# Kernel tuning notes

Measured on AMD Instinct MI355X. Metric: run time of the kernel, lower is better.

Reference implementation:

```python
import jax, jax.numpy as jnp
import numpy as np

# ---- db6 filter bank (pywt conventions) ----
_REC_LO = np.array([0.11154074335008017, 0.4946238903983854, 0.7511339080215775,
                    0.3152503517092432, -0.22626469396516913, -0.12976686756709563,
                    0.09750160558707936, 0.02752286553001629, -0.031582039318031156,
                    0.0005538422009938016, 0.004777257511010651, -0.00107730108499558],
                   dtype=np.float32)
_REC_HI = _REC_LO[::-1].copy(); _REC_HI[1::2] *= -1.0          # qmf(rec_lo)
_DEC_LO = _REC_LO[::-1].copy()
_DEC_HI = _REC_HI[::-1].copy()
L = 12          # filter length
LEVEL = 8       # J
# pytorch_wavelets cross-correlates with dec[::-1] == true conv with dec.
# lax.conv_general_dilated is correlation, so analysis kernels = dec[::-1] = rec filters.
ANA = jnp.asarray(np.stack([_REC_LO, _REC_HI])[:, None, :])     # [2,1,L]
SYN = jnp.asarray(np.stack([_DEC_LO, _DEC_HI])[None, :, :])     # [1,2,L]


def dwt1d(x, J):
    """Multi-level DWT, mode='symmetric'. x: [B,C,N] -> (yl [B,C,m], [yh1..yhJ])."""
    B, C, N = x.shape
    lo = x.reshape(B * C, 1, N)
    highs = []
    for _ in range(J):
        n = lo.shape[-1]
        outlen = (n + L - 1) // 2                    # pywt dwt_coeff_len
        p = 2 * (outlen - 1) - n + L
        xp = jnp.pad(lo, ((0, 0), (0, 0), (p // 2, (p + 1) // 2)), mode='symmetric')
        y = jax.lax.conv_general_dilated(xp, ANA, (2,), 'VALID',
                                         dimension_numbers=('NCH', 'OIH', 'NCH'))
        lo = y[:, :1]
        highs.append(y[:, 1:].reshape(B, C, outlen))
    return lo.reshape(B, C, -1), highs


def idwt1d(yl, yhs):
    """Inverse of dwt1d. yl: [B,C,m], yhs list (level1..levelJ)."""
    B, C, _ = yl.shape
    lo = yl.reshape(B * C, 1, -1)
    pad = L - 1 - (L - 2)                            # torch convT padding L-2 -> lax pad 1
    for h in yhs[::-1]:
        h = h.reshape(B * C, 1, -1)
        if lo.shape[-1] > h.shape[-1]:               # 'unpad' extra sample
            lo = lo[..., :h.shape[-1]]
        xh = jnp.concatenate([lo, h], axis=1)        # [BC,2,n]
        lo = jax.lax.conv_general_dilated(xh, SYN, (1,), [(pad, pad)],
                                          lhs_dilation=(2,),
                                          dimension_numbers=('NCH', 'OIH', 'NCH'))
    return lo.reshape(B, C, -1)


def wno_forward(x, fc0_w, fc0_b, w1, w2, cw, cb, fc1_w, fc1_b, fc2_w, fc2_b):
    B, s, _ = x.shape
    grid = jnp.broadcast_to(jnp.linspace(0.0, 1.0, s, dtype=x.dtype)[None, :, None], (B, s, 1))
    v = jnp.concatenate([x, grid], axis=-1) @ fc0_w + fc0_b     # [B,s,W]
    v = v.transpose(0, 2, 1)                                     # [B,W,s]
    n_layers = w1.shape[0]
    for i in range(n_layers):
        yl, yhs = dwt1d(v, LEVEL)
        yl = jnp.einsum('bix,iox->box', yl, w1[i])               # mix approx coeffs
        yhs[-1] = jnp.einsum('bix,iox->box', yhs[-1], w2[i])     # mix finest-level detail
        x1 = idwt1d(yl, yhs)
        x2 = jnp.einsum('bis,io->bos', v, cw[i]) + cb[i][None, :, None]  # 1x1 conv
        v = x1 + x2
        if i < n_layers - 1:
            v = jax.nn.gelu(v, approximate=False)
    v = v.transpose(0, 2, 1)
    v = jax.nn.gelu(v @ fc1_w + fc1_b, approximate=False)
    return v @ fc2_w + fc2_b                                     # [B,s,1]


def setup_inputs() -> dict:
    key = jax.random.key(0)
    B, S, W, NL = 32, 8192, 64, 4
    n = S
    for _ in range(LEVEL):
        n = (n + L - 1) // 2
    modes = n                                                    # 42
    ks = jax.random.split(key, 12)
    scale = 1.0 / (W * W)
    return {
        'x': jax.random.normal(ks[0], (B, S, 1), jnp.float32),
        'fc0_w': jax.random.normal(ks[1], (2, W), jnp.float32) * 0.5,
        'fc0_b': jax.random.normal(ks[2], (W,), jnp.float32) * 0.1,
        'w1': scale * jax.random.uniform(ks[3], (NL, W, W, modes), jnp.float32),
        'w2': scale * jax.random.uniform(ks[4], (NL, W, W, modes), jnp.float32),
        'cw': jax.random.normal(ks[5], (NL, W, W), jnp.float32) * (1.0 / np.sqrt(W)),
        'cb': jax.random.normal(ks[6], (NL, W), jnp.float32) * 0.05,
        'fc1_w': jax.random.normal(ks[7], (W, 128), jnp.float32) * (1.0 / np.sqrt(W)),
        'fc1_b': jax.random.normal(ks[8], (128,), jnp.float32) * 0.05,
        'fc2_w': jax.random.normal(ks[9], (128, 1), jnp.float32) * (1.0 / np.sqrt(128.0)),
        'fc2_b': jax.random.normal(ks[10], (1,), jnp.float32) * 0.05,
    }


def reference(x, fc0_w, fc0_b, w1, w2, cw, cb, fc1_w, fc1_b, fc2_w, fc2_b):
    return wno_forward(x, fc0_w, fc0_b, w1, w2, cw, cb, fc1_w, fc1_b, fc2_w, fc2_b)
```

## Files before the change

### kernel.cpp

```cpp
#include <hip/hip_runtime.h>
#include <cmath>

#define BC 2048
#define S_LEN 8192
#define MODES 42
#define HTOT 8248
#define LO_STR 1036

static constexpr float C_LO[12] = {
  0.11154074335008017f, 0.4946238903983854f, 0.7511339080215775f,
  0.3152503517092432f, -0.22626469396516913f, -0.12976686756709563f,
  0.09750160558707936f, 0.02752286553001629f, -0.031582039318031156f,
  0.0005538422009938016f, 0.004777257511010651f, -0.00107730108499558f };

__device__ __forceinline__ float rec_lo_c(int k){ return C_LO[k]; }
__device__ __forceinline__ float rec_hi_c(int k){ float v = C_LO[11-k]; return (k&1)? -v : v; }
__device__ __forceinline__ float dec_lo_c(int k){ return C_LO[11-k]; }
__device__ __forceinline__ float dec_hi_c(int k){ float v = C_LO[k];    return (k&1)?  v : -v; }

__device__ __forceinline__ float erf_fast(float x){
  float ax = fabsf(x);
  float t  = __fdividef(1.0f, 1.0f + 0.3275911f * ax);
  float p  = ((((1.061405429f * t - 1.453152027f) * t) + 1.421413741f) * t - 0.284496736f) * t + 0.254829592f;
  float y  = 1.0f - p * t * __expf(-ax * ax);
  return copysignf(y, x);
}
__device__ __forceinline__ float gelu_f(float x){
  return 0.5f * x * (1.0f + erf_fast(x * 0.70710678118654752440f));
}

__device__ __forceinline__ int reflect_i(int t, int n){
  t = (t < 0) ? (-1 - t) : t;
  t = (t >= n) ? (2 * n - 1 - t) : t;
  return t;
}

__device__ __forceinline__ unsigned short bf16_rn(float x){
  unsigned int b = __float_as_uint(x);
  b += 0x7FFF + ((b >> 16) & 1);
  return (unsigned short)(b >> 16);
}
__device__ __forceinline__ float bf16_to_f(unsigned short h){
  return __uint_as_float(((unsigned int)h) << 16);
}

typedef short  v8s __attribute__((ext_vector_type(8)));
typedef float  v4f __attribute__((ext_vector_type(4)));
typedef unsigned short u16;

__device__ __forceinline__ void ld3f4(float* w, const float* s){
  *(float4*)&w[0] = *(const float4*)&s[0];
  *(float4*)&w[4] = *(const float4*)&s[4];
  *(float4*)&w[8] = *(const float4*)&s[8];
}
__device__ __forceinline__ void ld5f4(float* w, const float* s){
  *(float4*)&w[0]  = *(const float4*)&s[0];
  *(float4*)&w[4]  = *(const float4*)&s[4];
  *(float4*)&w[8]  = *(const float4*)&s[8];
  *(float4*)&w[12] = *(const float4*)&s[12];
  *(float4*)&w[16] = *(const float4*)&s[16];
}

__device__ __forceinline__ void stage_g(float* dst, const float* src, int g0, int cnt, int n){
  for (int j4 = threadIdx.x; j4 < (cnt >> 2); j4 += 256) {
    int g = g0 + 4 * j4;
    float4 val;
    if (g >= 0 && g + 3 < n) val = *(const float4*)&src[g];
    else {
      val.x = (g   >= 0 && g   < n) ? src[g]   : 0.f;
      val.y = (g+1 >= 0 && g+1 < n) ? src[g+1] : 0.f;
      val.z = (g+2 >= 0 && g+2 < n) ? src[g+2] : 0.f;
      val.w = (g+3 >= 0 && g+3 < n) ? src[g+3] : 0.f;
    }
    *(float4*)&dst[4*j4] = val;
  }
}

template<int OFF>
__device__ __forceinline__ float idwt_tap(const float* wl, const float* wh, int d){
  float acc = 0.f;
  int t = OFF + (d >> 1);
  if (d & 1) {
    #pragma unroll
    for (int i = 0; i < 6; ++i) acc += wl[t+i]*dec_lo_c(2*i)   + wh[t+i]*dec_hi_c(2*i);
  } else {
    #pragma unroll
    for (int i = 0; i < 6; ++i) acc += wl[t+i]*dec_lo_c(2*i+1) + wh[t+i]*dec_hi_c(2*i+1);
  }
  return acc;
}

__global__ __launch_bounds__(256) void prep_split(
    const float* __restrict__ fc1w, const float* __restrict__ cw,
    u16* __restrict__ whH, u16* __restrict__ whL,
    u16* __restrict__ wcH, u16* __restrict__ wcL)
{
  int i = blockIdx.x * 256 + threadIdx.x;
  if (i < 8192) {
    int c = i >> 7, j = i & 127;
    float wv = fc1w[i];
    u16 h = bf16_rn(wv);
    float lo = wv - bf16_to_f(h);
    int cs = c ^ ((j & 7) << 3);
    whH[j * 64 + cs] = h; whL[j * 64 + cs] = bf16_rn(lo);
  }
  int k = i - 8192;
  if (k >= 0 && k < 16384) {
    int l = k >> 12, r = k & 4095;
    int c = r >> 6, o = r & 63;
    float wv = cw[k];
    u16 h = bf16_rn(wv);
    float lo = wv - bf16_to_f(h);
    int cs = c ^ ((o & 7) << 3);
    wcH[l * 4096 + o * 64 + cs] = h; wcL[l * 4096 + o * 64 + cs] = bf16_rn(lo);
  }
}

__global__ __launch_bounds__(256) void fc0_kernel(
    const float* __restrict__ x, const float* __restrict__ w,
    const float* __restrict__ bias, float* __restrict__ v)
{
  int p = blockIdx.x * 256 + threadIdx.x;
  int b = p >> 13, s = p & 8191;
  float xv = x[p];
  float g  = (float)s * (1.0f / 8191.0f);
  for (int c = 0; c < 64; ++c) {
    v[((size_t)(b * 64 + c)) * S_LEN + s] = xv * w[c] + g * w[64 + c] + bias[c];
  }
}

__global__ __launch_bounds__(256) void dwt_big(
    const float* __restrict__ vin, float* __restrict__ highs, float* __restrict__ lo_f)
{
  __shared__ alignas(16) float sV[2184], sL1[1088], sL2[544];
  int seq = blockIdx.x >> 2, c = blockIdx.x & 3;
  const float* src = vin + (size_t)seq * S_LEN;
  float* hseq = highs + (size_t)seq * HTOT;
  int tid = threadIdx.x;

  int g0 = 2080 * c - 72;
  for (int j4 = tid; j4 < 545; j4 += 256) {
    int g = g0 + 4 * j4;
    float4 val;
    if (g >= 0 && g + 3 < 8192) val = *(const float4*)&src[g];
    else {
      val.x = src[reflect_i(g,   8192)];
      val.y = src[reflect_i(g+1, 8192)];
      val.z = src[reflect_i(g+2, 8192)];
      val.w = src[reflect_i(g+3, 8192)];
    }
    *(float4*)&sV[4*j4] = val;
  }
  __syncthreads();

  int base1 = 1040 * c - 30;
  for (int u0 = 4*tid; u0 < 1082; u0 += 1024) {
    float w[20];
    ld5f4(w, &sV[2*u0]);
    #pragma unroll
    for (int d = 0; d < 4; ++d) {
      if (u0 + d < 1082) {
        float alo = 0.f, ahi = 0.f;
        #pragma unroll
        for (int k = 0; k < 12; ++k) {
          float x = w[2*d + 2 + k];
          alo += x * rec_lo_c(k); ahi += x * rec_hi_c(k);
        }
        sL1[u0+d] = alo;
        int m1 = base1 + u0 + d;
        if (m1 >= 1040*c && m1 < 1040*c + 1040 && m1 >= 0 && m1 < 4101) hseq[m1] = ahi;
      }
    }
  }
  __syncthreads();
  if (c == 0) { for (int u = tid;        u < 30;   u += 256) sL1[u] = sL1[59 - u]; }
  if (c == 3) { for (int u = 1011 + tid; u < 1082; u += 256) sL1[u] = sL1[2021 - u]; }
  __syncthreads();

  int base2 = 520 * c - 10;
  for (int u0 = 4*tid; u0 < 534; u0 += 1024) {
    float w[20];
    ld5f4(w, &sL1[2*u0]);
    #pragma unroll
    for (int d = 0; d < 4; ++d) {
      if (u0 + d < 534) {
        float alo = 0.f, ahi = 0.f;
        #pragma unroll
        for (int k = 0; k < 12; ++k) {
          float x = w[2*d + k];
          alo += x * rec_lo_c(k); ahi += x * rec_hi_c(k);
        }
        sL2[u0+d] = alo;
        int m2 = base2 + u0 + d;
        if (m2 >= 520*c && m2 < 520*c + 520 && m2 >= 0 && m2 < 2056) hseq[4104 + m2] = ahi;
      }
    }
  }
  __syncthreads();
  if (c == 0) { for (int u = tid;       u < 10;  u += 256) sL2[u] = sL2[19 - u]; }
  if (c == 3) { for (int u = 506 + tid; u < 534; u += 256) sL2[u] = sL2[1011 - u]; }
  __syncthreads();

  for (int u0 = 4*tid; u0 < 260; u0 += 1024) {
    float w[20];
    ld5f4(w, &sL2[2*u0]);
    #pragma unroll
    for (int d = 0; d < 4; ++d) {
      int m3 = 260*c + u0 + d;
      if (u0 + d < 260 && m3 < 1033) {
        float alo = 0.f, ahi = 0.f;
        #pragma unroll
        for (int k = 0; k < 12; ++k) {
          float x = w[2*d + k];
          alo += x * rec_lo_c(k); ahi += x * rec_hi_c(k);
        }
        lo_f[(size_t)seq * LO_STR + m3] = alo;
        hseq[6160 + m3] = ahi;
      }
    }
  }
}

__device__ __forceinline__ void dwt_lvl_v(const float* in, int n, float* out, int outn, float* hg)
{
  for (int u0 = 4*(int)threadIdx.x; u0 < outn; u0 += 1024) {
    bool fast = (u0 >= 8) && (2*u0 + 7 < n) && (u0 + 3 < outn);
    if (fast) {
      float w[20];
      ld5f4(w, &in[2*u0 - 12]);
      #pragma unroll
      for (int d = 0; d < 4; ++d) {
        float alo = 0.f, ahi = 0.f;
        #pragma unroll
        for (int k = 0; k < 12; ++k) {
          float x = w[2*d + 2 + k];
          alo += x * rec_lo_c(k); ahi += x * rec_hi_c(k);
        }
        out[u0+d] = alo; hg[u0+d] = ahi;
      }
    } else {
      for (int d = 0; d < 4; ++d) {
        if (u0 + d < outn) {
          float alo = 0.f, ahi = 0.f;
          #pragma unroll
          for (int k = 0; k < 12; ++k) {
            float x = in[reflect_i(2*(u0+d) + k - 10, n)];
            alo += x * rec_lo_c(k); ahi += x * rec_hi_c(k);
          }
          out[u0+d] = alo; hg[u0+d] = ahi;
        }
      }
    }
  }
  __syncthreads();
}

__global__ __launch_bounds__(256) void dwt_small(
    const float* __restrict__ lo_f, float* __restrict__ highs, float* __restrict__ yl)
{
  __shared__ alignas(16) float A[1040], Bb[528];
  int seq = blockIdx.x;
  const float* src = lo_f + (size_t)seq * LO_STR;
  float* hseq = highs + (size_t)seq * HTOT;
  for (int i = 4*(int)threadIdx.x; i < 1033; i += 1024) {
    if (i + 3 < 1033) *(float4*)&A[i] = *(const float4*)&src[i];
    else { for (int d = 0; d < 4; ++d) if (i + d < 1033) A[i+d] = src[i+d]; }
  }
  __syncthreads();
  dwt_lvl_v(A, 1033, Bb, 522, hseq + 7196);
  dwt_lvl_v(Bb, 522, A, 266, hseq + 7720);
  dwt_lvl_v(A, 266, Bb, 138, hseq + 7988);
  dwt_lvl_v(Bb, 138, A, 74,  hseq + 8128);
  dwt_lvl_v(A, 74,  Bb, 42,  hseq + 8204);
  for (int m = threadIdx.x; m < MODES; m += 256) yl[seq * MODES + m] = Bb[m];
}

__global__ __launch_bounds__(256) void mix2(
    const float* __restrict__ yl_raw, const float* __restrict__ highs,
    const float* __restrict__ w1i, const float* __restrict__ w2i,
    float* __restrict__ yl_m, float* __restrict__ yh_m)
{
  bool hi = blockIdx.x >= 336;
  int idx = (blockIdx.x - (hi ? 336 : 0)) * 256 + threadIdx.x;
  if (idx >= 32 * 64 * MODES) return;
  int xx = idx % MODES;
  int o  = (idx / MODES) % 64;
  int b  = idx / (MODES * 64);
  const float* in = hi ? (highs + 8204) : yl_raw;
  size_t stride   = hi ? HTOT : MODES;
  const float* w  = hi ? w2i : w1i;
  float acc = 0.f;
  for (int i = 0; i < 64; ++i)
    acc += in[((size_t)(b * 64 + i)) * stride + xx] * w[(i * 64 + o) * MODES + xx];
  (hi ? yh_m : yl_m)[(b * 64 + o) * MODES + xx] = acc;
}

__device__ __forceinline__ void idwt_lvl8(const float* lo, const float* h, float* out, int outn)
{
  for (int u0 = 8*(int)threadIdx.x; u0 < outn; u0 += 2048) {
    int ib = u0 >> 1;
    float wl[12], wh[12];
    ld3f4(wl, &lo[ib]); ld3f4(wh, &h[ib]);
    #pragma unroll
    for (int d = 0; d < 8; ++d)
      if (u0 + d < outn) out[u0+d] = idwt_tap<0>(wl, wh, d);
  }
  __syncthreads();
}

__device__ __forceinline__ void stage_band(float* dst, const float* src, int len, int alloc)
{
  for (int i = threadIdx.x; i < alloc; i += 256) dst[i] = (i < len) ? src[i] : 0.f;
}

__global__ __launch_bounds__(256) void idwt_small(
    const float* __restrict__ yl_m, const float* __restrict__ yh_m,
    const float* __restrict__ highs, float* __restrict__ lo_i)
{
  __shared__ alignas(16) float bands[1120], wa[272], wb[528];
  int seq = blockIdx.x;
  const float* hseq = highs + (size_t)seq * HTOT;
  stage_band(bands + 0,   yl_m + (size_t)seq * MODES, 42, 48);
  stage_band(bands + 48,  yh_m + (size_t)seq * MODES, 42, 48);
  stage_band(bands + 96,  hseq + 8128, 74, 80);
  stage_band(bands + 176, hseq + 7988, 138, 144);
  stage_band(bands + 320, hseq + 7720, 266, 272);
  stage_band(bands + 592, hseq + 7196, 522, 528);
  __syncthreads();
  idwt_lvl8(bands + 0,  bands + 48,  wa, 74);
  idwt_lvl8(wa,         bands + 96,  wb, 138);
  idwt_lvl8(wb,         bands + 176, wa, 266);
  idwt_lvl8(wa,         bands + 320, wb, 522);
  for (int u0 = 8*(int)threadIdx.x; u0 < 1033; u0 += 2048) {
    int ib = u0 >> 1;
    float wl[12], wh[12];
    ld3f4(wl, &wb[ib]); ld3f4(wh, &bands[592 + ib]);
    float o[8];
    #pragma unroll
    for (int d = 0; d < 8; ++d) o[d] = idwt_tap<0>(wl, wh, d);
    float* dst = lo_i + (size_t)seq * LO_STR + u0;
    if (u0 + 7 < 1033) {
      *(float4*)&dst[0] = make_float4(o[0], o[1], o[2], o[3]);
      *(float4*)&dst[4] = make_float4(o[4], o[5], o[6], o[7]);
    } else {
      for (int d = 0; d < 8; ++d) if (u0 + d < 1033) dst[d] = o[d];
    }
  }
}

__global__ __launch_bounds__(256) void idwt_big(
    const float* __restrict__ lo_i, const float* __restrict__ highs, float* __restrict__ x1)
{
  __shared__ alignas(16) float sL3[288], sH3[288], sL2[544], sH2[544], sL1[1048], sH1[1048];
  int seq = blockIdx.x >> 2, c = blockIdx.x & 3;
  const float* hseq = highs + (size_t)seq * HTOT;
  const float* l3   = lo_i + (size_t)seq * LO_STR;
  int g3 = 256*c - 4, g2 = 512*c - 4, g1 = 1024*c - 4;

  stage_g(sL3, l3,          g3, 288, 1033);
  stage_g(sH3, hseq + 6160, g3, 288, 1033);
  stage_g(sH2, hseq + 4104, g2, 544, 2056);
  stage_g(sH1, hseq,        g1, 1048, 4101);
  __syncthreads();

  for (int u0 = 8*(int)threadIdx.x; u0 < 536; u0 += 2048) {
    int ib = u0 >> 1;
    float wl[12], wh[12];
    ld3f4(wl, &sL3[ib]); ld3f4(wh, &sH3[ib]);
    #pragma unroll
    for (int d = 0; d < 8; ++d) {
      if (u0 + d < 536) {
        int m = 512*c - 2 + u0 + d;
        float acc = idwt_tap<3>(wl, wh, d);
        sL2[u0 + d + 2] = (m >= 0 && m < 2056) ? acc : 0.f;
      }
    }
  }
  __syncthreads();

  for (int u0 = 8*(int)threadIdx.x; u0 < 1040; u0 += 2048) {
    int ib = u0 >> 1;
    float wl[12], wh[12];
    ld3f4(wl, &sL2[ib]); ld3f4(wh, &sH2[ib]);
    #pragma unroll
    for (int d = 0; d < 8; ++d) {
      if (u0 + d < 1040) {
        int m = 1024*c - 2 + u0 + d;
        float acc = idwt_tap<3>(wl, wh, d);
        sL1[u0 + d + 2] = (m >= 0 && m < 4101) ? acc : 0.f;
      }
    }
  }
  __syncthreads();

  {
    int u0 = 8*(int)threadIdx.x;
    int ib = (u0 >> 1) + 4;
    float wl[12], wh[12];
    ld3f4(wl, &sL1[ib]); ld3f4(wh, &sH1[ib]);
    float o[8];
    #pragma unroll
    for (int d = 0; d < 8; ++d) o[d] = idwt_tap<0>(wl, wh, d);
    float* dst = x1 + (size_t)seq * S_LEN + 2048*c + u0;
    *(float4*)&dst[0] = make_float4(o[0], o[1], o[2], o[3]);
    *(float4*)&dst[4] = make_float4(o[4], o[5], o[6], o[7]);
  }
}

__global__ __launch_bounds__(256) void pw_mfma(
    const float* __restrict__ x1, float* v,
    const u16* __restrict__ wcH, const u16* __restrict__ wcL,
    const float* __restrict__ cb, int do_gelu)
{
  __shared__ u16 aH[64][64], aL[64][64];
  __shared__ u16 wH[64][64], wL[64][64];
  __shared__ float cbl[64];
  int b  = blockIdx.x >> 7;
  int s0 = (blockIdx.x & 127) << 6;
  int t  = threadIdx.x;

  {
    const v8s* srcH = (const v8s*)wcH;
    const v8s* srcL = (const v8s*)wcL;
    v8s* dstH = (v8s*)&wH[0][0];
    v8s* dstL = (v8s*)&wL[0][0];
    #pragma unroll
    for (int r = 0; r < 2; ++r) {
      dstH[t + 256 * r] = srcH[t + 256 * r];
      dstL[t + 256 * r] = srcL[t + 256 * r];
    }
  }
  if (t < 64) cbl[t] = cb[t];

  #pragma unroll
  for (int r = 0; r < 4; ++r) {
    int idx = t + 256 * r;
    int ch = idx >> 4, p4 = (idx & 15) << 2;
    float4 xv = *(const float4*)&v[((size_t)(b * 64 + ch)) * S_LEN + s0 + p4];
    u16 h0 = bf16_rn(xv.x); aH[p4+0][ch ^ (((p4+0)&7)<<3)] = h0; aL[p4+0][ch ^ (((p4+0)&7)<<3)] = bf16_rn(xv.x - bf16_to_f(h0));
    u16 h1 = bf16_rn(xv.y); aH[p4+1][ch ^ (((p4+1)&7)<<3)] = h1; aL[p4+1][ch ^ (((p4+1)&7)<<3)] = bf16_rn(xv.y - bf16_to_f(h1));
    u16 h2 = bf16_rn(xv.z); aH[p4+2][ch ^ (((p4+2)&7)<<3)] = h2; aL[p4+2][ch ^ (((p4+2)&7)<<3)] = bf16_rn(xv.z - bf16_to_f(h2));
    u16 h3 = bf16_rn(xv.w); aH[p4+3][ch ^ (((p4+3)&7)<<3)] = h3; aL[p4+3][ch ^ (((p4+3)&7)<<3)] = bf16_rn(xv.w - bf16_to_f(h3));
  }
  __syncthreads();

  int l = t & 63, wv_ = t >> 6;
  int pi = l & 15, kg = l >> 4;
  int pos = wv_ * 16 + pi;
  int swz = (pi & 7) << 3;

  v4f acc[4];
  #pragma unroll
  for (int i = 0; i < 4; ++i) acc[i] = v4f{0.f, 0.f, 0.f, 0.f};

  #pragma unroll
  for (int kt = 0; kt < 2; ++kt) {
    int ka = (kg * 8 + kt * 32) ^ swz;
    v8s ah = *(const v8s*)&aH[pos][ka];
    v8s al = *(const v8s*)&aL[pos][ka];
    #pragma unroll
    for (int ct = 0; ct < 4; ++ct) {
      int o = ct * 16 + pi;
      v8s bh = *(const v8s*)&wH[o][ka];
      v8s bl = *(const v8s*)&wL[o][ka];
      acc[ct] = __builtin_amdgcn_mfma_f32_16x16x32_bf16(ah, bh, acc[ct], 0, 0, 0);
      acc[ct] = __builtin_amdgcn_mfma_f32_16x16x32_bf16(ah, bl, acc[ct], 0, 0, 0);
      acc[ct] = __builtin_amdgcn_mfma_f32_16x16x32_bf16(al, bh, acc[ct], 0, 0, 0);
    }
  }

  #pragma unroll
  for (int ct = 0; ct < 4; ++ct) {
    int o = ct * 16 + pi;
    size_t base = ((size_t)(b * 64 + o)) * S_LEN + s0 + wv_ * 16 + kg * 4;
    float4 x4 = *(const float4*)&x1[base];
    float cbv = cbl[o];
    float y0 = acc[ct][0] + x4.x + cbv;
    float y1 = acc[ct][1] + x4.y + cbv;
    float y2 = acc[ct][2] + x4.z + cbv;
    float y3 = acc[ct][3] + x4.w + cbv;
    if (do_gelu) { y0 = gelu_f(y0); y1 = gelu_f(y1); y2 = gelu_f(y2); y3 = gelu_f(y3); }
    float4 y4 = make_float4(y0, y1, y2, y3);
    *(float4*)&v[base] = y4;
  }
}

__global__ __launch_bounds__(256) void head_mfma(
    const float* __restrict__ v,
    const u16* __restrict__ whH, const u16* __restrict__ whL,
    const float* __restrict__ fc1b, const float* __restrict__ fc2w,
    const float* __restrict__ fc2b, float* __restrict__ out)
{
  __shared__ u16 aH[64][64], aL[64][64];
  __shared__ u16 wH[128][64], wL[128][64];
  __shared__ float f1b[128], f2w[128];
  int b  = blockIdx.x >> 7;
  int s0 = (blockIdx.x & 127) << 6;
  int t  = threadIdx.x;

  {
    const v8s* srcH = (const v8s*)whH;
    const v8s* srcL = (const v8s*)whL;
    v8s* dstH = (v8s*)&wH[0][0];
    v8s* dstL = (v8s*)&wL[0][0];
    #pragma unroll
    for (int r = 0; r < 4; ++r) {
      dstH[t + 256 * r] = srcH[t + 256 * r];
      dstL[t + 256 * r] = srcL[t + 256 * r];
    }
  }
  if (t < 128) { f1b[t] = fc1b[t]; f2w[t] = fc2w[t]; }

  #pragma unroll
  for (int r = 0; r < 4; ++r) {
    int idx = t + 256 * r;
    int ch = idx >> 4, p4 = (idx & 15) << 2;
    float4 xv = *(const float4*)&v[((size_t)(b * 64 + ch)) * S_LEN + s0 + p4];
    u16 h0 = bf16_rn(xv.x); aH[p4+0][ch ^ (((p4+0)&7)<<3)] = h0; aL[p4+0][ch ^ (((p4+0)&7)<<3)] = bf16_rn(xv.x - bf16_to_f(h0));
    u16 h1 = bf16_rn(xv.y); aH[p4+1][ch ^ (((p4+1)&7)<<3)] = h1; aL[p4+1][ch ^ (((p4+1)&7)<<3)] = bf16_rn(xv.y - bf16_to_f(h1));
    u16 h2 = bf16_rn(xv.z); aH[p4+2][ch ^ (((p4+2)&7)<<3)] = h2; aL[p4+2][ch ^ (((p4+2)&7)<<3)] = bf16_rn(xv.z - bf16_to_f(h2));
    u16 h3 = bf16_rn(xv.w); aH[p4+3][ch ^ (((p4+3)&7)<<3)] = h3; aL[p4+3][ch ^ (((p4+3)&7)<<3)] = bf16_rn(xv.w - bf16_to_f(h3));
  }
  __syncthreads();

  int l = t & 63, wv_ = t >> 6;
  int pi = l & 15, kg = l >> 4;
  int pos = wv_ * 16 + pi;
  int swz = (pi & 7) << 3;

  v4f acc[8];
  #pragma unroll
  for (int i = 0; i < 8; ++i) acc[i] = v4f{0.f, 0.f, 0.f, 0.f};

  #pragma unroll
  for (int kt = 0; kt < 2; ++kt) {
    int ka = (kg * 8 + kt * 32) ^ swz;
    v8s ah = *(const v8s*)&aH[pos][ka];
    v8s al = *(const v8s*)&aL[pos][ka];
    #pragma unroll
    for (int ct = 0; ct < 8; ++ct) {
      int j = ct * 16 + pi;
      v8s bh = *(const v8s*)&wH[j][ka];
      v8s bl = *(const v8s*)&wL[j][ka];
      acc[ct] = __builtin_amdgcn_mfma_f32_16x16x32_bf16(ah, bh, acc[ct], 0, 0, 0);
      acc[ct] = __builtin_amdgcn_mfma_f32_16x16x32_bf16(ah, bl, acc[ct], 0, 0, 0);
      acc[ct] = __builtin_amdgcn_mfma_f32_16x16x32_bf16(al, bh, acc[ct], 0, 0, 0);
    }
  }

  float part[4] = {0.f, 0.f, 0.f, 0.f};
  #pragma unroll
  for (int ct = 0; ct < 8; ++ct) {
    int j = ct * 16 + pi;
    float bias = f1b[j], f2 = f2w[j];
    #pragma unroll
    for (int r = 0; r < 4; ++r) {
      float d = acc[ct][r] + bias;
      part[r] += f2 * gelu_f(d);
    }
  }
  #pragma unroll
  for (int r = 0; r < 4; ++r) {
    part[r] += __shfl_xor(part[r], 1, 16);
    part[r] += __shfl_xor(part[r], 2, 16);
    part[r] += __shfl_xor(part[r], 4, 16);
    part[r] += __shfl_xor(part[r], 8, 16);
  }
  if (pi == 0) {
    float b2 = fc2b[0];
    float4 o4 = make_float4(part[0] + b2, part[1] + b2, part[2] + b2, part[3] + b2);
    *(float4*)&out[(size_t)b * S_LEN + s0 + wv_ * 16 + kg * 4] = o4;
  }
}

extern "C" void kernel_launch(void* const* d_in, const int* in_sizes, int n_in,
                              void* d_out, int out_size, void* d_ws, size_t ws_size,
                              hipStream_t stream) {
  const float* x    = (const float*)d_in[0];
  const float* fc0w = (const float*)d_in[1];
  const float* fc0b = (const float*)d_in[2];
  const float* w1   = (const float*)d_in[3];
  const float* w2   = (const float*)d_in[4];
  const float* cw   = (const float*)d_in[5];
  const float* cb   = (const float*)d_in[6];
  const float* fc1w = (const float*)d_in[7];
  const float* fc1b = (const float*)d_in[8];
  const float* fc2w = (const float*)d_in[9];
  const float* fc2b = (const float*)d_in[10];
  float* out = (float*)d_out;

  float* ws     = (float*)d_ws;
  float* v      = ws;
  float* x1     = v      + (size_t)BC * S_LEN;
  float* highs  = x1     + (size_t)BC * S_LEN;
  float* yl_raw = highs  + (size_t)BC * HTOT;
  float* yl_m   = yl_raw + (size_t)BC * MODES;
  float* yh_m   = yl_m   + (size_t)BC * MODES;
  float* lo_f   = yh_m   + (size_t)BC * MODES;
  float* lo_i   = lo_f   + (size_t)BC * LO_STR;
  u16*   whH    = (u16*)(lo_i + (size_t)BC * LO_STR);
  u16*   whL    = whH + 8192;
  u16*   wcH    = whL + 8192;
  u16*   wcL    = wcH + 16384;
  size_t needed = (size_t)((char*)(wcL + 16384) - (char*)ws);
  if (ws_size < needed) return;

  prep_split<<<96, 256, 0, stream>>>(fc1w, cw, whH, whL, wcH, wcL);
  fc0_kernel<<<1024, 256, 0, stream>>>(x, fc0w, fc0b, v);

  for (int i = 0; i < 4; ++i) {
    dwt_big<<<BC * 4, 256, 0, stream>>>(v, highs, lo_f);
    dwt_small<<<BC, 256, 0, stream>>>(lo_f, highs, yl_raw);
    mix2<<<672, 256, 0, stream>>>(yl_raw, highs, w1 + (size_t)i * 64 * 64 * MODES,
                                  w2 + (size_t)i * 64 * 64 * MODES, yl_m, yh_m);
    idwt_small<<<BC, 256, 0, stream>>>(yl_m, yh_m, highs, lo_i);
    idwt_big<<<BC * 4, 256, 0, stream>>>(lo_i, highs, x1);
    pw_mfma<<<4096, 256, 0, stream>>>(x1, v, wcH + i * 4096, wcL + i * 4096, cb + i * 64, (i < 3) ? 1 : 0);
  }

  head_mfma<<<4096, 256, 0, stream>>>(v, whH, whL, fc1b, fc2w, fc2b, out);
}
```

Before: 610.1 us.

## Fuse mode mixing into idwt_small and deinterleave DWT shared buffers

The separate mix2 kernel goes away. Its per-mode channel contraction is now done inside idwt_small, with each block computing its own output channel's 42 low and high modes before the inverse transform. dwt_big now keeps even and odd samples in separate shared arrays, so strided filter reads become contiguous vector loads, and it writes high bands with float4 stores. The idwt kernels drop from 8 to 4 outputs per thread to cut register pressure. The fused mixing work runs on only 42 threads per block and re-reads weights for every (b,o), which may serialize or add global traffic.

```diff
diff --git a/kernel.cpp b/kernel.cpp
--- a/kernel.cpp
+++ b/kernel.cpp
@@ -59,6 +59,12 @@
   *(float4*)&w[8]  = *(const float4*)&s[8];
   *(float4*)&w[12] = *(const float4*)&s[12];
   *(float4*)&w[16] = *(const float4*)&s[16];
+}
+__device__ __forceinline__ void ld4f2(float* w, const float* s){
+  *(float2*)&w[0] = *(const float2*)&s[0];
+  *(float2*)&w[2] = *(const float2*)&s[2];
+  *(float2*)&w[4] = *(const float2*)&s[4];
+  *(float2*)&w[6] = *(const float2*)&s[6];
 }
 
 __device__ __forceinline__ void stage_g(float* dst, const float* src, int g0, int cnt, int n){
@@ -76,18 +82,36 @@
   }
 }
 
-template<int OFF>
-__device__ __forceinline__ float idwt_tap(const float* wl, const float* wh, int d){
-  float acc = 0.f;
-  int t = OFF + (d >> 1);
-  if (d & 1) {
-    #pragma unroll
-    for (int i = 0; i < 6; ++i) acc += wl[t+i]*dec_lo_c(2*i)   + wh[t+i]*dec_hi_c(2*i);
-  } else {
-    #pragma unroll
-    for (int i = 0; i < 6; ++i) acc += wl[t+i]*dec_lo_c(2*i+1) + wh[t+i]*dec_hi_c(2*i+1);
-  }
-  return acc;
+__device__ __forceinline__ void stage_band4(float* dst, const float* src, int len, int alloc){
+  for (int i4 = threadIdx.x; i4 < (alloc >> 2); i4 += 256) {
+    int i = 4 * i4;
+    float4 v;
+    if (i + 3 < len) v = *(const float4*)&src[i];
+    else {
+      v.x = (i   < len) ? src[i]   : 0.f;
+      v.y = (i+1 < len) ? src[i+1] : 0.f;
+      v.z = (i+2 < len) ? src[i+2] : 0.f;
+      v.w = (i+3 < len) ? src[i+3] : 0.f;
+    }
+    *(float4*)&dst[i] = v;
+  }
+}
+
+template<int SH>
+__device__ __forceinline__ void idwt4s(const float* wl, const float* wh, float* o4){
+  #pragma unroll
+  for (int d = 0; d < 4; ++d) {
+    const int q = SH + (d >> 1);
+    float acc = 0.f;
+    if (d & 1) {
+      #pragma unroll
+      for (int i = 0; i < 6; ++i) acc += wl[q+i]*dec_lo_c(2*i)   + wh[q+i]*dec_hi_c(2*i);
+    } else {
+      #pragma unroll
+      for (int i = 0; i < 6; ++i) acc += wl[q+i]*dec_lo_c(2*i+1) + wh[q+i]*dec_hi_c(2*i+1);
+    }
+    o4[d] = acc;
+  }
 }
 
 __global__ __launch_bounds__(256) void prep_split(
@@ -132,13 +156,18 @@
 __global__ __launch_bounds__(256) void dwt_big(
     const float* __restrict__ vin, float* __restrict__ highs, float* __restrict__ lo_f)
 {
-  __shared__ alignas(16) float sV[2184], sL1[1088], sL2[544];
+  __shared__ alignas(16) float sVE[1096], sVO[1096];
+  __shared__ alignas(16) float sL1Eb[548], sL1Ob[548];
+  __shared__ alignas(16) float sL2E[276], sL2O[276];
+  float* sL1E = sL1Eb + 4;
+  float* sL1O = sL1Ob + 4;
+
   int seq = blockIdx.x >> 2, c = blockIdx.x & 3;
   const float* src = vin + (size_t)seq * S_LEN;
   float* hseq = highs + (size_t)seq * HTOT;
   int tid = threadIdx.x;
 
-  int g0 = 2080 * c - 72;
+  int g0 = 2080 * c - 76;
   for (int j4 = tid; j4 < 545; j4 += 256) {
     int g = g0 + 4 * j4;
     float4 val;
@@ -149,73 +178,127 @@
       val.z = src[reflect_i(g+2, 8192)];
       val.w = src[reflect_i(g+3, 8192)];
     }
-    *(float4*)&sV[4*j4] = val;
-  }
-  __syncthreads();
-
-  int base1 = 1040 * c - 30;
-  for (int u0 = 4*tid; u0 < 1082; u0 += 1024) {
-    float w[20];
-    ld5f4(w, &sV[2*u0]);
-    #pragma unroll
-    for (int d = 0; d < 4; ++d) {
-      if (u0 + d < 1082) {
+    *(float2*)&sVE[2*j4] = make_float2(val.x, val.z);
+    *(float2*)&sVO[2*j4] = make_float2(val.y, val.w);
+  }
+  __syncthreads();
+
+  {
+    int base1m = 1040 * c - 32;
+    int uh1 = (c < 3) ? 1072 : 1013;
+    for (int u0 = 4 * tid; u0 < 1084; u0 += 1024) {
+      float we[12], wo[12];
+      ld3f4(we, &sVE[u0]); ld3f4(wo, &sVO[u0]);
+      float lo4[4], hi4[4];
+      #pragma unroll
+      for (int d = 0; d < 4; ++d) {
         float alo = 0.f, ahi = 0.f;
         #pragma unroll
-        for (int k = 0; k < 12; ++k) {
-          float x = w[2*d + 2 + k];
-          alo += x * rec_lo_c(k); ahi += x * rec_hi_c(k);
+        for (int j = 0; j < 6; ++j) {
+          float e = we[d+1+j], oo = wo[d+1+j];
+          alo += e * rec_lo_c(2*j) + oo * rec_lo_c(2*j+1);
+          ahi += e * rec_hi_c(2*j) + oo * rec_hi_c(2*j+1);
         }
-        sL1[u0+d] = alo;
-        int m1 = base1 + u0 + d;
-        if (m1 >= 1040*c && m1 < 1040*c + 1040 && m1 >= 0 && m1 < 4101) hseq[m1] = ahi;
+        lo4[d] = alo; hi4[d] = ahi;
       }
-    }
-  }
-  __syncthreads();
-  if (c == 0) { for (int u = tid;        u < 30;   u += 256) sL1[u] = sL1[59 - u]; }
-  if (c == 3) { for (int u = 1011 + tid; u < 1082; u += 256) sL1[u] = sL1[2021 - u]; }
-  __syncthreads();
-
-  int base2 = 520 * c - 10;
-  for (int u0 = 4*tid; u0 < 534; u0 += 1024) {
-    float w[20];
-    ld5f4(w, &sL1[2*u0]);
-    #pragma unroll
-    for (int d = 0; d < 4; ++d) {
-      if (u0 + d < 534) {
+      *(float2*)&sL1E[u0 >> 1] = make_float2(lo4[0], lo4[2]);
+      *(float2*)&sL1O[u0 >> 1] = make_float2(lo4[1], lo4[3]);
+      if (u0 >= 32 && u0 + 3 < uh1) {
+        *(float4*)&hseq[base1m + u0] = make_float4(hi4[0], hi4[1], hi4[2], hi4[3]);
+      } else {
+        #pragma unroll
+        for (int d = 0; d < 4; ++d) {
+          int u = u0 + d;
+          if (u >= 32 && u < uh1) hseq[base1m + u] = hi4[d];
+        }
+      }
+    }
+  }
+  __syncthreads();
+  if (c == 0) {
+    for (int u = tid; u < 32; u += 256) {
+      int j = 63 - u;
+      float v = (j & 1) ? sL1O[j >> 1] : sL1E[j >> 1];
+      if (u & 1) sL1O[u >> 1] = v; else sL1E[u >> 1] = v;
+    }
+  }
+  if (c == 3) {
+    for (int u = 1013 + tid; u < 1084; u += 256) {
+      int j = 2025 - u;
+      float v = (j & 1) ? sL1O[j >> 1] : sL1E[j >> 1];
+      if (u & 1) sL1O[u >> 1] = v; else sL1E[u >> 1] = v;
+    }
+  }
+  __syncthreads();
+
+  {
+    int base2m = 520 * c - 12;
+    int uh2 = (c < 3) ? 532 : 508;
+    for (int u0 = 4 * tid; u0 < 536; u0 += 1024) {
+      float we[12], wo[12];
+      ld3f4(we, &sL1E[u0 - 4]); ld3f4(wo, &sL1O[u0 - 4]);
+      float lo4[4], hi4[4];
+      #pragma unroll
+      for (int d = 0; d < 4; ++d) {
         float alo = 0.f, ahi = 0.f;
         #pragma unroll
-        for (int k = 0; k < 12; ++k) {
-          float x = w[2*d + k];
-          alo += x * rec_lo_c(k); ahi += x * rec_hi_c(k);
+        for (int j = 0; j < 6; ++j) {
+          float e = we[d+3+j], oo = wo[d+3+j];
+          alo += e * rec_lo_c(2*j) + oo * rec_lo_c(2*j+1);
+          ahi += e * rec_hi_c(2*j) + oo * rec_hi_c(2*j+1);
         }
-        sL2[u0+d] = alo;
-        int m2 = base2 + u0 + d;
-        if (m2 >= 520*c && m2 < 520*c + 520 && m2 >= 0 && m2 < 2056) hseq[4104 + m2] = ahi;
+        lo4[d] = alo; hi4[d] = ahi;
       }
-    }
-  }
-  __syncthreads();
-  if (c == 0) { for (int u = tid;       u < 10;  u += 256) sL2[u] = sL2[19 - u]; }
-  if (c == 3) { for (int u = 506 + tid; u < 534; u += 256) sL2[u] = sL2[1011 - u]; }
-  __syncthreads();
-
-  for (int u0 = 4*tid; u0 < 260; u0 += 1024) {
-    float w[20];
-    ld5f4(w, &sL2[2*u0]);
+      *(float2*)&sL2E[u0 >> 1] = make_float2(lo4[0], lo4[2]);
+      *(float2*)&sL2O[u0 >> 1] = make_float2(lo4[1], lo4[3]);
+      if (u0 >= 12 && u0 < uh2)
+        *(float4*)&hseq[4104 + base2m + u0] = make_float4(hi4[0], hi4[1], hi4[2], hi4[3]);
+    }
+  }
+  __syncthreads();
+  if (c == 0) {
+    for (int u = tid; u < 12; u += 256) {
+      int j = 23 - u;
+      float v = (j & 1) ? sL2O[j >> 1] : sL2E[j >> 1];
+      if (u & 1) sL2O[u >> 1] = v; else sL2E[u >> 1] = v;
+    }
+  }
+  if (c == 3) {
+    for (int u = 508 + tid; u < 536; u += 256) {
+      int j = 1015 - u;
+      float v = (j & 1) ? sL2O[j >> 1] : sL2E[j >> 1];
+      if (u & 1) sL2O[u >> 1] = v; else sL2E[u >> 1] = v;
+    }
+  }
+  __syncthreads();
+
+  for (int u0 = 4 * tid; u0 < 260; u0 += 1024) {
+    float we[12], wo[12];
+    ld3f4(we, &sL2E[u0]); ld3f4(wo, &sL2O[u0]);
+    float lo4[4], hi4[4];
     #pragma unroll
     for (int d = 0; d < 4; ++d) {
-      int m3 = 260*c + u0 + d;
-      if (u0 + d < 260 && m3 < 1033) {
-        float alo = 0.f, ahi = 0.f;
-        #pragma unroll
-        for (int k = 0; k < 12; ++k) {
-          float x = w[2*d + k];
-          alo += x * rec_lo_c(k); ahi += x * rec_hi_c(k);
+      float alo = 0.f, ahi = 0.f;
+      #pragma unroll
+      for (int j = 0; j < 6; ++j) {
+        float e = we[d+1+j], oo = wo[d+1+j];
+        alo += e * rec_lo_c(2*j) + oo * rec_lo_c(2*j+1);
+        ahi += e * rec_hi_c(2*j) + oo * rec_hi_c(2*j+1);
+      }
+      lo4[d] = alo; hi4[d] = ahi;
+    }
+    int m0 = 260 * c + u0;
+    if (m0 + 3 < 1033) {
+      *(float4*)&lo_f[(size_t)seq * LO_STR + m0] = make_float4(lo4[0], lo4[1], lo4[2], lo4[3]);
+      *(float4*)&hseq[6160 + m0] = make_float4(hi4[0], hi4[1], hi4[2], hi4[3]);
+    } else {
+      #pragma unroll
+      for (int d = 0; d < 4; ++d) {
+        int m = m0 + d;
+        if (m < 1033 && u0 + d < 260) {
+          lo_f[(size_t)seq * LO_STR + m] = lo4[d];
+          hseq[6160 + m] = hi4[d];
         }
-        lo_f[(size_t)seq * LO_STR + m3] = alo;
-        hseq[6160 + m3] = ahi;
       }
     }
   }
@@ -275,76 +358,64 @@
   for (int m = threadIdx.x; m < MODES; m += 256) yl[seq * MODES + m] = Bb[m];
 }
 
-__global__ __launch_bounds__(256) void mix2(
+__device__ __forceinline__ void idwt_lvl4(const float* lo, const float* h, float* out, int outn)
+{
+  for (int u0 = 4*(int)threadIdx.x; u0 < outn; u0 += 1024) {
+    int q = u0 >> 1;
+    float wl[8], wh[8];
+    ld4f2(wl, &lo[q]); ld4f2(wh, &h[q]);
+    float o4[4]; idwt4s<0>(wl, wh, o4);
+    if (u0 + 3 < outn) *(float4*)&out[u0] = make_float4(o4[0], o4[1], o4[2], o4[3]);
+    else { for (int d = 0; d < 4; ++d) if (u0 + d < outn) out[u0+d] = o4[d]; }
+  }
+  __syncthreads();
+}
+
+__global__ __launch_bounds__(256) void idwt_small(
     const float* __restrict__ yl_raw, const float* __restrict__ highs,
-    const float* __restrict__ w1i, const float* __restrict__ w2i,
-    float* __restrict__ yl_m, float* __restrict__ yh_m)
-{
-  bool hi = blockIdx.x >= 336;
-  int idx = (blockIdx.x - (hi ? 336 : 0)) * 256 + threadIdx.x;
-  if (idx >= 32 * 64 * MODES) return;
-  int xx = idx % MODES;
-  int o  = (idx / MODES) % 64;
-  int b  = idx / (MODES * 64);
-  const float* in = hi ? (highs + 8204) : yl_raw;
-  size_t stride   = hi ? HTOT : MODES;
-  const float* w  = hi ? w2i : w1i;
-  float acc = 0.f;
-  for (int i = 0; i < 64; ++i)
-    acc += in[((size_t)(b * 64 + i)) * stride + xx] * w[(i * 64 + o) * MODES + xx];
-  (hi ? yh_m : yl_m)[(b * 64 + o) * MODES + xx] = acc;
-}
-
-__device__ __forceinline__ void idwt_lvl8(const float* lo, const float* h, float* out, int outn)
-{
-  for (int u0 = 8*(int)threadIdx.x; u0 < outn; u0 += 2048) {
-    int ib = u0 >> 1;
-    float wl[12], wh[12];
-    ld3f4(wl, &lo[ib]); ld3f4(wh, &h[ib]);
-    #pragma unroll
-    for (int d = 0; d < 8; ++d)
-      if (u0 + d < outn) out[u0+d] = idwt_tap<0>(wl, wh, d);
-  }
-  __syncthreads();
-}
-
-__device__ __forceinline__ void stage_band(float* dst, const float* src, int len, int alloc)
-{
-  for (int i = threadIdx.x; i < alloc; i += 256) dst[i] = (i < len) ? src[i] : 0.f;
-}
-
-__global__ __launch_bounds__(256) void idwt_small(
-    const float* __restrict__ yl_m, const float* __restrict__ yh_m,
-    const float* __restrict__ highs, float* __restrict__ lo_i)
+    const float* __restrict__ w1l, const float* __restrict__ w2l,
+    float* __restrict__ lo_i)
 {
   __shared__ alignas(16) float bands[1120], wa[272], wb[528];
   int seq = blockIdx.x;
+  int b = seq >> 6, o = seq & 63;
   const float* hseq = highs + (size_t)seq * HTOT;
-  stage_band(bands + 0,   yl_m + (size_t)seq * MODES, 42, 48);
-  stage_band(bands + 48,  yh_m + (size_t)seq * MODES, 42, 48);
-  stage_band(bands + 96,  hseq + 8128, 74, 80);
-  stage_band(bands + 176, hseq + 7988, 138, 144);
-  stage_band(bands + 320, hseq + 7720, 266, 272);
-  stage_band(bands + 592, hseq + 7196, 522, 528);
-  __syncthreads();
-  idwt_lvl8(bands + 0,  bands + 48,  wa, 74);
-  idwt_lvl8(wa,         bands + 96,  wb, 138);
-  idwt_lvl8(wb,         bands + 176, wa, 266);
-  idwt_lvl8(wa,         bands + 320, wb, 522);
-  for (int u0 = 8*(int)threadIdx.x; u0 < 1033; u0 += 2048) {
-    int ib = u0 >> 1;
-    float wl[12], wh[12];
-    ld3f4(wl, &wb[ib]); ld3f4(wh, &bands[592 + ib]);
-    float o[8];
-    #pragma unroll
-    for (int d = 0; d < 8; ++d) o[d] = idwt_tap<0>(wl, wh, d);
+  int t = threadIdx.x;
+
+  stage_band4(bands + 96,  hseq + 8128, 74, 80);
+  stage_band4(bands + 176, hseq + 7988, 138, 144);
+  stage_band4(bands + 320, hseq + 7720, 266, 272);
+  stage_band4(bands + 592, hseq + 7196, 522, 528);
+
+  if (t >= 42 && t < 48) { bands[t] = 0.f; bands[48 + t] = 0.f; }
+  if (t < 42) {
+    const float* yr = yl_raw + (size_t)b * 2688 + t;
+    const float* hh = highs + (size_t)(b * 64) * HTOT + 8204 + t;
+    const float* wl = w1l + o * 42 + t;
+    const float* wh = w2l + o * 42 + t;
+    float accl = 0.f, acch = 0.f;
+    #pragma unroll 4
+    for (int i = 0; i < 64; ++i) {
+      accl += yr[i * 42] * wl[i * 2688];
+      acch += hh[(size_t)i * HTOT] * wh[i * 2688];
+    }
+    bands[t] = accl; bands[48 + t] = acch;
+  }
+  __syncthreads();
+
+  idwt_lvl4(bands + 0,   bands + 48,  wa, 74);
+  idwt_lvl4(wa,          bands + 96,  wb, 138);
+  idwt_lvl4(wb,          bands + 176, wa, 266);
+  idwt_lvl4(wa,          bands + 320, wb, 522);
+
+  for (int u0 = 4 * t; u0 < 1033; u0 += 1024) {
+    int q = u0 >> 1;
+    float wl[8], wh[8];
+    ld4f2(wl, &wb[q]); ld4f2(wh, &bands[592 + q]);
+    float o4[4]; idwt4s<0>(wl, wh, o4);
     float* dst = lo_i + (size_t)seq * LO_STR + u0;
-    if (u0 + 7 < 1033) {
-      *(float4*)&dst[0] = make_float4(o[0], o[1], o[2], o[3]);
-      *(float4*)&dst[4] = make_float4(o[4], o[5], o[6], o[7]);
-    } else {
-      for (int d = 0; d < 8; ++d) if (u0 + d < 1033) dst[d] = o[d];
-    }
+    if (u0 + 3 < 1033) *(float4*)&dst[0] = make_float4(o4[0], o4[1], o4[2], o4[3]);
+    else { for (int d = 0; d < 4; ++d) if (u0 + d < 1033) dst[d] = o4[d]; }
   }
 }
 
@@ -356,6 +427,7 @@
   const float* hseq = highs + (size_t)seq * HTOT;
   const float* l3   = lo_i + (size_t)seq * LO_STR;
   int g3 = 256*c - 4, g2 = 512*c - 4, g1 = 1024*c - 4;
+  int t = threadIdx.x;
 
   stage_g(sL3, l3,          g3, 288, 1033);
   stage_g(sH3, hseq + 6160, g3, 288, 1033);
@@ -363,47 +435,42 @@
   stage_g(sH1, hseq,        g1, 1048, 4101);
   __syncthreads();
 
-  for (int u0 = 8*(int)threadIdx.x; u0 < 536; u0 += 2048) {
-    int ib = u0 >> 1;
-    float wl[12], wh[12];
-    ld3f4(wl, &sL3[ib]); ld3f4(wh, &sH3[ib]);
-    #pragma unroll
-    for (int d = 0; d < 8; ++d) {
-      if (u0 + d < 536) {
-        int m = 512*c - 2 + u0 + d;
-        float acc = idwt_tap<3>(wl, wh, d);
-        sL2[u0 + d + 2] = (m >= 0 && m < 2056) ? acc : 0.f;
-      }
-    }
-  }
-  __syncthreads();
-
-  for (int u0 = 8*(int)threadIdx.x; u0 < 1040; u0 += 2048) {
-    int ib = u0 >> 1;
-    float wl[12], wh[12];
-    ld3f4(wl, &sL2[ib]); ld3f4(wh, &sH2[ib]);
-    #pragma unroll
-    for (int d = 0; d < 8; ++d) {
-      if (u0 + d < 1040) {
-        int m = 1024*c - 2 + u0 + d;
-        float acc = idwt_tap<3>(wl, wh, d);
-        sL1[u0 + d + 2] = (m >= 0 && m < 4101) ? acc : 0.f;
-      }
-    }
-  }
-  __syncthreads();
-
-  {
-    int u0 = 8*(int)threadIdx.x;
-    int ib = (u0 >> 1) + 4;
-    float wl[12], wh[12];
-    ld3f4(wl, &sL1[ib]); ld3f4(wh, &sH1[ib]);
-    float o[8];
-    #pragma unroll
-    for (int d = 0; d < 8; ++d) o[d] = idwt_tap<0>(wl, wh, d);
-    float* dst = x1 + (size_t)seq * S_LEN + 2048*c + u0;
-    *(float4*)&dst[0] = make_float4(o[0], o[1], o[2], o[3]);
-    *(float4*)&dst[4] = make_float4(o[4], o[5], o[6], o[7]);
+  for (int u0 = 4 * t; u0 < 536; u0 += 1024) {
+    int q = u0 >> 1;
+    float wl[8], wh[8];
+    ld4f2(wl, &sL3[q + 2]); ld4f2(wh, &sH3[q + 2]);
+    float o4[4]; idwt4s<1>(wl, wh, o4);
+    #pragma unroll
+    for (int d = 0; d < 4; ++d) {
+      int m = 512*c - 2 + u0 + d;
+      o4[d] = (m >= 0 && m < 2056) ? o4[d] : 0.f;
+    }
+    *(float2*)&sL2[u0 + 2] = make_float2(o4[0], o4[1]);
+    *(float2*)&sL2[u0 + 4] = make_float2(o4[2], o4[3]);
+  }
+  __syncthreads();
+
+  for (int u0 = 4 * t; u0 < 1040; u0 += 1024) {
+    int q = u0 >> 1;
+    float wl[8], wh[8];
+    ld4f2(wl, &sL2[q + 2]); ld4f2(wh, &sH2[q + 2]);
+    float o4[4]; idwt4s<1>(wl, wh, o4);
+    #pragma unroll
+    for (int d = 0; d < 4; ++d) {
+      int m = 1024*c - 2 + u0 + d;
+      o4[d] = (m >= 0 && m < 4101) ? o4[d] : 0.f;
+    }
+    *(float2*)&sL1[u0 + 2] = make_float2(o4[0], o4[1]);
+    *(float2*)&sL1[u0 + 4] = make_float2(o4[2], o4[3]);
+  }
+  __syncthreads();
+
+  for (int u0 = 4 * t; u0 < 2048; u0 += 1024) {
+    int q = u0 >> 1;
+    float wl[8], wh[8];
+    ld4f2(wl, &sL1[q + 4]); ld4f2(wh, &sH1[q + 4]);
+    float o4[4]; idwt4s<0>(wl, wh, o4);
+    *(float4*)&x1[(size_t)seq * S_LEN + 2048*c + u0] = make_float4(o4[0], o4[1], o4[2], o4[3]);
   }
 }
 
@@ -594,9 +661,7 @@
   float* x1     = v      + (size_t)BC * S_LEN;
   float* highs  = x1     + (size_t)BC * S_LEN;
   float* yl_raw = highs  + (size_t)BC * HTOT;
-  float* yl_m   = yl_raw + (size_t)BC * MODES;
-  float* yh_m   = yl_m   + (size_t)BC * MODES;
-  float* lo_f   = yh_m   + (size_t)BC * MODES;
+  float* lo_f   = yl_raw + (size_t)BC * MODES;
   float* lo_i   = lo_f   + (size_t)BC * LO_STR;
   u16*   whH    = (u16*)(lo_i + (size_t)BC * LO_STR);
   u16*   whL    = whH + 8192;
@@ -609,11 +674,11 @@
   fc0_kernel<<<1024, 256, 0, stream>>>(x, fc0w, fc0b, v);
 
   for (int i = 0; i < 4; ++i) {
+    const float* w1l = w1 + (size_t)i * 64 * 64 * MODES;
+    const float* w2l = w2 + (size_t)i * 64 * 64 * MODES;
     dwt_big<<<BC * 4, 256, 0, stream>>>(v, highs, lo_f);
     dwt_small<<<BC, 256, 0, stream>>>(lo_f, highs, yl_raw);
-    mix2<<<672, 256, 0, stream>>>(yl_raw, highs, w1 + (size_t)i * 64 * 64 * MODES,
-                                  w2 + (size_t)i * 64 * 64 * MODES, yl_m, yh_m);
-    idwt_small<<<BC, 256, 0, stream>>>(yl_m, yh_m, highs, lo_i);
+    idwt_small<<<BC, 256, 0, stream>>>(yl_raw, highs, w1l, w2l, lo_i);
     idwt_big<<<BC * 4, 256, 0, stream>>>(lo_i, highs, x1);
     pw_mfma<<<4096, 256, 0, stream>>>(x1, v, wcH + i * 4096, wcL + i * 4096, cb + i * 64, (i < 3) ? 1 : 0);
   }
```

After: 584.6 us. 1.04x faster.
